# Performance work log

Hardware: AMD Instinct MI355X
Metric: run time of the kernel (lower is better)

The kernel has to match this reference:

```python
import jax, jax.numpy as jnp
import numpy as np
from jax import lax


def setup_inputs() -> dict:
    key = jax.random.key(0)
    ks = jax.random.split(key, 16)
    def rn(k, shape, s=0.05):
        return (jax.random.normal(k, shape) * s).astype(jnp.float32)
    B, N, F = 16, 1024, 200
    return dict(
        x=jax.random.normal(ks[0], (B, 1, N, F), dtype=jnp.float32),
        gat_W=rn(ks[1], (F, F)), att_src=rn(ks[2], (F,)), att_dst=rn(ks[3], (F,)), gat_b=rn(ks[4], (F,)),
        conv1_w=rn(ks[5], (40, 1, 1, 26)), conv1_b=rn(ks[6], (40,)),
        bn1_g=jnp.ones((40,), jnp.float32), bn1_b=jnp.zeros((40,), jnp.float32),
        bn1_m=jnp.zeros((40,), jnp.float32), bn1_v=jnp.ones((40,), jnp.float32),
        conv2_w=rn(ks[7], (40, 40, N), 0.01), conv2_b=rn(ks[8], (40,)),
        bn2_g=jnp.ones((40,), jnp.float32), bn2_b=jnp.zeros((40,), jnp.float32),
        bn2_m=jnp.zeros((40,), jnp.float32), bn2_v=jnp.ones((40,), jnp.float32),
        projc_w=rn(ks[9], (40, 40)), projc_b=rn(ks[10], (40,)),
        W1=rn(ks[11], (1400, 1024)), b1=rn(ks[12], (1024,)),
        W2=rn(ks[13], (1024, 1024)), b2=rn(ks[14], (1024,)),
        ln_g=jnp.ones((1024,), jnp.float32), ln_b=jnp.zeros((1024,), jnp.float32),
    )


def _bn(y, g, b, m, v, eps=1e-5):
    # eval-mode BatchNorm over channel axis 1
    shp = (1, -1) + (1,) * (y.ndim - 2)
    return (y - m.reshape(shp)) * (g.reshape(shp) / jnp.sqrt(v.reshape(shp) + eps)) + b.reshape(shp)


def reference(x, gat_W, att_src, att_dst, gat_b, conv1_w, conv1_b,
              bn1_g, bn1_b, bn1_m, bn1_v, conv2_w, conv2_b,
              bn2_g, bn2_b, bn2_m, bn2_v, projc_w, projc_b,
              W1, b1, W2, b2, ln_g, ln_b):
    B, _, N, F = x.shape  # (16,1,1024,200)
    # --- EEG_GAT (PyG GATConv, heads=1). edge_index only covers nodes 0..N-1;
    # add_self_loops applies to all B*N nodes -> first graph is dense attention
    # (complete graph incl. self), remaining nodes see only their self-loop.
    h = x.reshape(B * N, F) @ gat_W               # (B*N, 200)
    a_s = h[:N] @ att_src                          # source scores, first graph
    a_d = h[:N] @ att_dst                          # target scores
    logits = jax.nn.leaky_relu(a_s[None, :] + a_d[:, None], 0.2)  # [target i, source j]
    out0 = jax.nn.softmax(logits, axis=1) @ h[:N]  # (N, 200)
    gat = (jnp.concatenate([out0, h[N:]], axis=0) + gat_b).reshape(B, 1, N, F)
    x = x + gat  # ResidualAdd (dropout in eval = identity)
    # --- PatchEmbedding shallownet
    y = lax.conv_general_dilated(x, conv1_w, (1, 1), 'VALID',
                                 dimension_numbers=('NCHW', 'OIHW', 'NCHW'))
    y = y + conv1_b[None, :, None, None]           # (B,40,1024,175)
    y = y.reshape(B, 40, N, 35, 5).mean(-1)        # AvgPool2d (1,5) stride (1,5)
    y = jax.nn.elu(_bn(y, bn1_g, bn1_b, bn1_m, bn1_v))
    y = jnp.einsum('bchw,och->bow', y, conv2_w) + conv2_b[None, :, None]  # Conv2d(40,40,(1024,1)) -> (B,40,35)
    y = jax.nn.elu(_bn(y, bn2_g, bn2_b, bn2_m, bn2_v))
    # projection 1x1 conv then rearrange 'b e h w -> b (h w) e' then flatten
    y = jnp.einsum('bow,eo->bew', y, projc_w) + projc_b[None, :, None]
    y = y.transpose(0, 2, 1).reshape(B, -1)        # (B, 1400)
    # --- Proj_eeg
    z = y @ W1 + b1
    z = z + (jax.nn.gelu(z, approximate=False) @ W2 + b2)
    mu = z.mean(-1, keepdims=True)
    var = ((z - mu) ** 2).mean(-1, keepdims=True)
    return (z - mu) / jnp.sqrt(var + 1e-5) * ln_g + ln_b
```

## Files before the change

kernel.cpp:

```cpp
#include <hip/hip_runtime.h>
#include <math.h>

typedef __attribute__((ext_vector_type(8))) short short8;
typedef __attribute__((ext_vector_type(4))) float f32x4;

__device__ __forceinline__ unsigned f2bf(float f) {
  unsigned u = __float_as_uint(f);
  return (u + 0x7FFFu + ((u >> 16) & 1u)) >> 16;
}
__device__ __forceinline__ unsigned pk2(float lo, float hi) {
  return f2bf(lo) | (f2bf(hi) << 16);
}

#define WS_X1    0
#define WS_W2P   3328000
#define WS_AS    4966400
#define WS_AD    4967424
#define WS_WEFF  4968464
#define WS_S1    4969664
#define WS_SH1   4969704
#define WS_S2    4969744
#define WS_SH2   4969784
#define WS_H     4970496
#define WS_P     5232640
#define WS_AP    6281216
#define WS_Y3P   WS_P
#define WS_Y4    8378368
#define WS_Y5    8400768
#define WS_ZP    8455936
#define WS_Z2P   8570624
#define WS_WPT   8701696

__global__ __launch_bounds__(256) void k0_prep(const float* __restrict__ gat_W,
                        const float* __restrict__ conv1_w, const float* __restrict__ conv1_b,
                        const float* __restrict__ bn1_g, const float* __restrict__ bn1_b,
                        const float* __restrict__ bn1_m, const float* __restrict__ bn1_v,
                        const float* __restrict__ conv2_b,
                        const float* __restrict__ bn2_g, const float* __restrict__ bn2_b,
                        const float* __restrict__ bn2_m, const float* __restrict__ bn2_v,
                        const float* __restrict__ w2,
                        float* __restrict__ ws) {
  int bx = blockIdx.x, t = threadIdx.x;
  if (bx < 224) {
    unsigned short* wpt = (unsigned short*)(ws + WS_WPT);
    int idx = bx * 256 + t;
    int n = idx / 224, k = idx % 224;
    float v = (n < 200 && k < 200) ? gat_W[k * 200 + n] : 0.f;
    wpt[idx] = (unsigned short)f2bf(v);
    return;
  }
  if (bx == 224) {
    if (t < 40) {
      float* weff = ws + WS_WEFF;
      for (int j = 0; j < 30; ++j) {
        float s = 0.f;
        for (int tt = 0; tt < 5; ++tt) {
          int k = j - tt;
          if (k >= 0 && k < 26) s += conv1_w[t * 26 + k];
        }
        weff[t * 30 + j] = s * 0.2f;
      }
      float s1 = bn1_g[t] * rsqrtf(bn1_v[t] + 1e-5f);
      ws[WS_S1 + t] = s1;
      ws[WS_SH1 + t] = bn1_b[t] + (conv1_b[t] - bn1_m[t]) * s1;
      float s2 = bn2_g[t] * rsqrtf(bn2_v[t] + 1e-5f);
      ws[WS_S2 + t] = s2;
      ws[WS_SH2 + t] = bn2_b[t] + (conv2_b[t] - bn2_m[t]) * s2;
    }
    return;
  }
  int idx = (bx - 225) * 256 + t;
  if (idx < 1966080) {
    unsigned short* w2p = (unsigned short*)(ws + WS_W2P);
    int k = idx % 320;
    int rem = idx / 320;
    int o = rem % 48, c8 = rem / 48;
    float v = 0.f;
    if (o < 40) {
      int c = k % 40, nl = k / 40;
      v = w2[(o * 40 + c) * 1024 + c8 * 8 + nl];
    }
    w2p[idx] = (unsigned short)f2bf(v);
  }
}

__global__ __launch_bounds__(256) void k1_mfma(const float* __restrict__ x,
                                               const unsigned short* __restrict__ wpt,
                                               const float* __restrict__ gat_b,
                                               float* __restrict__ h,
                                               float* __restrict__ x1) {
  __shared__ unsigned short Bt[64 * 232];
  __shared__ unsigned short As[2][64 * 40];
  int t = threadIdx.x;
  int wave = t >> 6, lane = t & 63;
  int m16 = lane & 15, quad = lane >> 4;
  int row0 = blockIdx.x * 64, n0 = blockIdx.y * 64;
  for (int i = t; i < 1792; i += 256) {
    int row = i / 28, ch = i % 28;
    *(short8*)&Bt[row * 232 + ch * 8] = *(const short8*)&wpt[(n0 + row) * 224 + ch * 8];
  }
  {
    int m = t >> 2, kq = (t & 3) * 8;
    const float* xr = x + (row0 + m) * 200 + kq;
    float4 a = *(const float4*)xr;
    float4 b = *(const float4*)(xr + 4);
    uint4 pv;
    pv.x = pk2(a.x, a.y); pv.y = pk2(a.z, a.w);
    pv.z = pk2(b.x, b.y); pv.w = pk2(b.z, b.w);
    *(uint4*)&As[0][m * 40 + kq] = pv;
  }
  __syncthreads();
  f32x4 acc0 = {0.f, 0.f, 0.f, 0.f}, acc1 = acc0, acc2 = acc0, acc3 = acc0;
  int buf = 0;
  for (int s = 0; s < 7; ++s) {
    if (s < 6) {
      int m = t >> 2, kq = (t & 3) * 8;
      int kg = (s + 1) * 32 + kq;
      const float* xr = x + (row0 + m) * 200;
      uint4 pv;
      if (kg + 8 <= 200) {
        float4 a = *(const float4*)(xr + kg);
        float4 b = *(const float4*)(xr + kg + 4);
        pv.x = pk2(a.x, a.y); pv.y = pk2(a.z, a.w);
        pv.z = pk2(b.x, b.y); pv.w = pk2(b.z, b.w);
      } else {
        float e[8];
#pragma unroll
        for (int q = 0; q < 8; ++q) e[q] = (kg + q < 200) ? xr[kg + q] : 0.f;
        pv.x = pk2(e[0], e[1]); pv.y = pk2(e[2], e[3]);
        pv.z = pk2(e[4], e[5]); pv.w = pk2(e[6], e[7]);
      }
      *(uint4*)&As[buf ^ 1][m * 40 + kq] = pv;
    }
    short8 af = *(const short8*)&As[buf][(wave * 16 + m16) * 40 + quad * 8];
    int kb = s * 32 + quad * 8;
    short8 b0 = *(const short8*)&Bt[(0 * 16 + m16) * 232 + kb];
    short8 b1 = *(const short8*)&Bt[(1 * 16 + m16) * 232 + kb];
    short8 b2 = *(const short8*)&Bt[(2 * 16 + m16) * 232 + kb];
    short8 b3 = *(const short8*)&Bt[(3 * 16 + m16) * 232 + kb];
    acc0 = __builtin_amdgcn_mfma_f32_16x16x32_bf16(af, b0, acc0, 0, 0, 0);
    acc1 = __builtin_amdgcn_mfma_f32_16x16x32_bf16(af, b1, acc1, 0, 0, 0);
    acc2 = __builtin_amdgcn_mfma_f32_16x16x32_bf16(af, b2, acc2, 0, 0, 0);
    acc3 = __builtin_amdgcn_mfma_f32_16x16x32_bf16(af, b3, acc3, 0, 0, 0);
    __syncthreads();
    buf ^= 1;
  }
  f32x4 accs[4] = {acc0, acc1, acc2, acc3};
  if (blockIdx.x < 16) {
#pragma unroll
    for (int nt = 0; nt < 4; ++nt)
#pragma unroll
      for (int r = 0; r < 4; ++r) {
        int row = row0 + wave * 16 + quad * 4 + r;
        h[row * 256 + n0 + nt * 16 + m16] = accs[nt][r];
      }
  } else {
#pragma unroll
    for (int nt = 0; nt < 4; ++nt) {
      int col = n0 + nt * 16 + m16;
      if (col < 200) {
#pragma unroll
        for (int r = 0; r < 4; ++r) {
          int row = row0 + wave * 16 + quad * 4 + r;
          x1[row * 200 + col] = x[row * 200 + col] + accs[nt][r] + gat_b[col];
        }
      }
    }
  }
}

__global__ void k1b_scores(const float* __restrict__ h, const float* __restrict__ att_src,
                           const float* __restrict__ att_dst, float* __restrict__ as_,
                           float* __restrict__ ad_) {
  int r = blockIdx.x * 256 + threadIdx.x;
  const float* hr = h + r * 256;
  float s = 0.f, d = 0.f;
  for (int f = 0; f < 200; ++f) {
    float v = hr[f];
    s += v * att_src[f];
    d += v * att_dst[f];
  }
  as_[r] = s;
  ad_[r] = d;
}

__global__ __launch_bounds__(256) void kP(const float* __restrict__ as_,
                                          const float* __restrict__ ad_,
                                          float* __restrict__ P) {
  __shared__ float rb[256];
  int t = threadIdx.x, i = blockIdx.x;
  float a0 = as_[t], a1 = as_[256 + t], a2 = as_[512 + t], a3 = as_[768 + t];
  rb[t] = fmaxf(fmaxf(a0, a1), fmaxf(a2, a3));
  __syncthreads();
  for (int st = 128; st > 0; st >>= 1) {
    if (t < st) rb[t] = fmaxf(rb[t], rb[t + st]);
    __syncthreads();
  }
  float maxs = rb[0];
  __syncthreads();
  float ad = ad_[i];
  float mv = maxs + ad;
  float M = mv >= 0.f ? mv : 0.2f * mv;
  float av[4] = {a0, a1, a2, a3};
  float p[4];
  float s = 0.f;
#pragma unroll
  for (int q = 0; q < 4; ++q) {
    float v = av[q] + ad;
    float l = v >= 0.f ? v : 0.2f * v;
    p[q] = __expf(l - M);
    s += p[q];
  }
  rb[t] = s;
  __syncthreads();
  for (int st = 128; st > 0; st >>= 1) {
    if (t < st) rb[t] += rb[t + st];
    __syncthreads();
  }
  float inv = 1.f / rb[0];
#pragma unroll
  for (int q = 0; q < 4; ++q) P[i * 1024 + q * 256 + t] = p[q] * inv;
}

__global__ __launch_bounds__(256) void kAttn(const float* __restrict__ P,
                                             const float* __restrict__ h,
                                             float* __restrict__ ap) {
  __shared__ __align__(16) float As2[8][64];
  __shared__ __align__(16) float Bs[8][64];
  int t = threadIdx.x;
  int tm = t & 15, tn = t >> 4;
  int i0 = blockIdx.x * 64, f0 = blockIdx.y * 64, j0 = blockIdx.z * 128;
  float acc[4][4] = {};
  for (int k0 = 0; k0 < 128; k0 += 8) {
    for (int i = t; i < 512; i += 256) {
      int m = i >> 3, k = i & 7;
      As2[k][m] = P[(i0 + m) * 1024 + j0 + k0 + k];
    }
    for (int i = t; i < 512; i += 256) {
      int k = i >> 6, n = i & 63;
      Bs[k][n] = h[(j0 + k0 + k) * 256 + f0 + n];
    }
    __syncthreads();
#pragma unroll
    for (int k = 0; k < 8; ++k) {
      float4 a = *(const float4*)&As2[k][tm * 4];
      float4 bq = *(const float4*)&Bs[k][tn * 4];
      float av[4] = {a.x, a.y, a.z, a.w};
      float bv[4] = {bq.x, bq.y, bq.z, bq.w};
#pragma unroll
      for (int i = 0; i < 4; ++i)
#pragma unroll
        for (int j = 0; j < 4; ++j) acc[i][j] += av[i] * bv[j];
    }
    __syncthreads();
  }
#pragma unroll
  for (int i = 0; i < 4; ++i) {
    int r = i0 + tm * 4 + i;
    float4 v = make_float4(acc[i][0], acc[i][1], acc[i][2], acc[i][3]);
    *(float4*)&ap[(blockIdx.z * 1024 + r) * 256 + f0 + tn * 4] = v;
  }
}

__global__ __launch_bounds__(256) void kAttnRed(const float* __restrict__ ap,
                                                const float* __restrict__ x,
                                                const float* __restrict__ gat_b,
                                                float* __restrict__ x1) {
  int t = threadIdx.x, r = blockIdx.x;
  if (t >= 200) return;
  float s = 0.f;
#pragma unroll
  for (int z = 0; z < 8; ++z) s += ap[(z * 1024 + r) * 256 + t];
  x1[r * 200 + t] = x[r * 200 + t] + s + gat_b[t];
}

__global__ __launch_bounds__(320, 2) void k3_conv(const float* __restrict__ x1,
                                                  const unsigned short* __restrict__ w2pre,
                                                  const float* __restrict__ ws,
                                                  float* __restrict__ y3p) {
  __shared__ __align__(16) char smem[33856];
  float* xbp = (float*)smem;
  unsigned short* tmpA = (unsigned short*)(smem + 10240);
  int t = threadIdx.x;
  int b = blockIdx.x, nc = blockIdx.y;
  int n0 = nc * 8;
  int wave = t >> 6, lane = t & 63;
  int l15 = lane & 15, quad = lane >> 4;
  for (int i = t; i < 400; i += 320) {
    int nn = i / 50, q = i % 50;
    float4 v = ((const float4*)(x1 + (b * 1024 + n0 + nn) * 200))[q];
    float vv[4] = {v.x, v.y, v.z, v.w};
#pragma unroll
    for (int m = 0; m < 4; ++m) {
      int j = q * 4 + m;
      xbp[nn * 320 + (j / 5) * 8 + (j % 5)] = vv[m];
    }
  }
  int c1 = t / 7, wg = t % 7;
  float wr[30];
  float s1c = 0.f, sh1c = 0.f;
  if (t < 280) {
    const float* weff = ws + WS_WEFF + c1 * 30;
#pragma unroll
    for (int j = 0; j < 30; ++j) wr[j] = weff[j];
    s1c = ws[WS_S1 + c1];
    sh1c = ws[WS_SH1 + c1];
  }
  __syncthreads();
  if (t < 280) {
    for (int nn = 0; nn < 8; ++nn) {
      float xq[10][5];
      int xb = nn * 320 + wg * 40;
#pragma unroll
      for (int pi = 0; pi < 10; ++pi) {
        float4 v = *(const float4*)&xbp[xb + pi * 8];
        xq[pi][0] = v.x; xq[pi][1] = v.y; xq[pi][2] = v.z; xq[pi][3] = v.w;
        xq[pi][4] = xbp[xb + pi * 8 + 4];
      }
#pragma unroll
      for (int u = 0; u < 5; ++u) {
        float s = 0.f;
#pragma unroll
        for (int m = 0; m < 6; ++m)
#pragma unroll
          for (int r = 0; r < 5; ++r) s += xq[u + m][r] * wr[m * 5 + r];
        float v = s * s1c + sh1c;
        float e = v > 0.f ? v : __expf(v) - 1.f;
        tmpA[(wg * 5 + u) * 328 + nn * 40 + c1] = (unsigned short)f2bf(e);
      }
    }
  }
  __syncthreads();
  f32x4 acc[3][3];
#pragma unroll
  for (int mt = 0; mt < 3; ++mt)
#pragma unroll
    for (int nt = 0; nt < 3; ++nt) acc[mt][nt] = (f32x4){0.f, 0.f, 0.f, 0.f};
  const unsigned short* bbase = w2pre + nc * 48 * 320;
#pragma unroll
  for (int ks = 0; ks < 2; ++ks) {
    int koff = wave * 64 + ks * 32 + quad * 8;
    short8 a[3], bb[3];
#pragma unroll
    for (int mt = 0; mt < 3; ++mt) {
      int row = mt * 16 + l15;
      row = row > 35 ? 35 : row;
      a[mt] = *(const short8*)&tmpA[row * 328 + koff];
    }
#pragma unroll
    for (int nt = 0; nt < 3; ++nt)
      bb[nt] = *(const short8*)&bbase[(nt * 16 + l15) * 320 + koff];
#pragma unroll
    for (int mt = 0; mt < 3; ++mt)
#pragma unroll
      for (int nt = 0; nt < 3; ++nt)
        acc[mt][nt] = __builtin_amdgcn_mfma_f32_16x16x32_bf16(a[mt], bb[nt], acc[mt][nt], 0, 0, 0);
  }
  __syncthreads();
  float* red0 = (float*)smem;
  float* red1 = red0 + 48 * 49;
  if (wave < 2) {
    float* r = wave ? red1 : red0;
#pragma unroll
    for (int mt = 0; mt < 3; ++mt)
#pragma unroll
      for (int nt = 0; nt < 3; ++nt)
#pragma unroll
        for (int q = 0; q < 4; ++q)
          r[(mt * 16 + quad * 4 + q) * 49 + nt * 16 + l15] = acc[mt][nt][q];
  }
  __syncthreads();
  if (wave == 2 || wave == 3) {
    float* r = (wave == 3) ? red1 : red0;
#pragma unroll
    for (int mt = 0; mt < 3; ++mt)
#pragma unroll
      for (int nt = 0; nt < 3; ++nt)
#pragma unroll
        for (int q = 0; q < 4; ++q)
          r[(mt * 16 + quad * 4 + q) * 49 + nt * 16 + l15] += acc[mt][nt][q];
  }
  __syncthreads();
  if (wave == 4) {
#pragma unroll
    for (int mt = 0; mt < 3; ++mt)
#pragma unroll
      for (int nt = 0; nt < 3; ++nt)
#pragma unroll
        for (int q = 0; q < 4; ++q)
          red0[(mt * 16 + quad * 4 + q) * 49 + nt * 16 + l15] += acc[mt][nt][q];
  }
  __syncthreads();
  float* dst = y3p + (b * 128 + nc) * 1400;
  for (int idx = t; idx < 1400; idx += 320) {
    int o = idx / 35, p = idx % 35;
    dst[idx] = red0[p * 49 + o] + red1[p * 49 + o];
  }
}

__global__ __launch_bounds__(256) void k4a_red(const float* __restrict__ y3p,
                                               const float* __restrict__ ws,
                                               float* __restrict__ y4) {
  int t = threadIdx.x;
  if (t >= 200) return;
  int b = blockIdx.x;
  int idx = blockIdx.y * 200 + t;
  float s = 0.f;
#pragma unroll 4
  for (int q = 0; q < 128; ++q) s += y3p[(b * 128 + q) * 1400 + idx];
  int o = idx / 35;
  float v = s * ws[WS_S2 + o] + ws[WS_SH2 + o];
  y4[b * 1400 + idx] = v > 0.f ? v : __expf(v) - 1.f;
}

__global__ __launch_bounds__(256) void k4b_proj(const float* __restrict__ y4,
                                                const float* __restrict__ projc_w,
                                                const float* __restrict__ projc_b,
                                                float* __restrict__ y5) {
  __shared__ __align__(16) float tls[1400];
  int t = threadIdx.x, b = blockIdx.x;
  for (int i = t; i < 350; i += 256)
    ((float4*)tls)[i] = ((const float4*)(y4 + b * 1400))[i];
  __syncthreads();
  for (int idx = t; idx < 1400; idx += 256) {
    int p = idx / 40, e = idx % 40;
    float acc = projc_b[e];
    for (int o = 0; o < 40; ++o) acc += tls[o * 35 + p] * projc_w[e * 40 + o];
    y5[b * 1400 + idx] = acc;
  }
}

__global__ __launch_bounds__(256) void k5_fc1(const float* __restrict__ y5,
                                              const float* __restrict__ W1,
                                              float* __restrict__ zp) {
  __shared__ __align__(16) float yls[3200];
  int t = threadIdx.x;
  int nc = blockIdx.x, kc = blockIdx.y;
  for (int i = t; i < 800; i += 256) {
    int bb = i / 50, q = i % 50;
    ((float4*)yls)[bb * 50 + q] = *(const float4*)(y5 + bb * 1400 + kc * 200 + q * 4);
  }
  __syncthreads();
  int nl = t & 31, bg = t >> 5;
  int n = nc * 32 + nl;
  float acc0 = 0.f, acc1 = 0.f;
  const float* y0 = yls + (bg * 2) * 200;
  const float* y1 = yls + (bg * 2 + 1) * 200;
  for (int k = 0; k < 200; ++k) {
    float w = W1[(kc * 200 + k) * 1024 + n];
    acc0 += y0[k] * w;
    acc1 += y1[k] * w;
  }
  zp[(kc * 16 + bg * 2) * 1024 + n] = acc0;
  zp[(kc * 16 + bg * 2 + 1) * 1024 + n] = acc1;
}

__global__ __launch_bounds__(256) void k6_fc2(const float* __restrict__ zp,
                                              const float* __restrict__ b1,
                                              const float* __restrict__ W2,
                                              float* __restrict__ z2p) {
  __shared__ __align__(16) float gls[2048];
  int t = threadIdx.x;
  int nc = blockIdx.x, kc = blockIdx.y;
  for (int i = t; i < 2048; i += 256) {
    int bb = i >> 7, kk = i & 127;
    int np = kc * 128 + kk;
    float s = b1[np];
#pragma unroll
    for (int j = 0; j < 7; ++j) s += zp[(j * 16 + bb) * 1024 + np];
    gls[i] = 0.5f * s * (1.f + erff(s * 0.70710678f));
  }
  __syncthreads();
  int nl = t & 31, bg = t >> 5;
  int n = nc * 32 + nl;
  float acc0 = 0.f, acc1 = 0.f;
  const float* g0 = gls + (bg * 2) * 128;
  const float* g1 = gls + (bg * 2 + 1) * 128;
  for (int k = 0; k < 128; ++k) {
    float w = W2[(kc * 128 + k) * 1024 + n];
    acc0 += g0[k] * w;
    acc1 += g1[k] * w;
  }
  z2p[(kc * 16 + bg * 2) * 1024 + n] = acc0;
  z2p[(kc * 16 + bg * 2 + 1) * 1024 + n] = acc1;
}

__global__ __launch_bounds__(256) void k7_ln(const float* __restrict__ zp,
                                             const float* __restrict__ z2p,
                                             const float* __restrict__ b1,
                                             const float* __restrict__ b2,
                                             const float* __restrict__ ln_g,
                                             const float* __restrict__ ln_b,
                                             float* __restrict__ out) {
  __shared__ float r1[256], r2[256];
  int t = threadIdx.x, b = blockIdx.x;
  float4 v = *(const float4*)(b1 + t * 4);
  float4 bb2 = *(const float4*)(b2 + t * 4);
  v.x += bb2.x; v.y += bb2.y; v.z += bb2.z; v.w += bb2.w;
#pragma unroll
  for (int kc = 0; kc < 7; ++kc) {
    float4 p = *(const float4*)(zp + (kc * 16 + b) * 1024 + t * 4);
    v.x += p.x; v.y += p.y; v.z += p.z; v.w += p.w;
  }
#pragma unroll
  for (int kc = 0; kc < 8; ++kc) {
    float4 p = *(const float4*)(z2p + (kc * 16 + b) * 1024 + t * 4);
    v.x += p.x; v.y += p.y; v.z += p.z; v.w += p.w;
  }
  r1[t] = v.x + v.y + v.z + v.w;
  r2[t] = v.x * v.x + v.y * v.y + v.z * v.z + v.w * v.w;
  __syncthreads();
  for (int s = 128; s > 0; s >>= 1) {
    if (t < s) {
      r1[t] += r1[t + s];
      r2[t] += r2[t + s];
    }
    __syncthreads();
  }
  float mu = r1[0] * (1.f / 1024.f);
  float var = r2[0] * (1.f / 1024.f) - mu * mu;
  float rstd = rsqrtf(var + 1e-5f);
  float4 gg = *(const float4*)(ln_g + t * 4);
  float4 bb = *(const float4*)(ln_b + t * 4);
  float4 o;
  o.x = (v.x - mu) * rstd * gg.x + bb.x;
  o.y = (v.y - mu) * rstd * gg.y + bb.y;
  o.z = (v.z - mu) * rstd * gg.z + bb.z;
  o.w = (v.w - mu) * rstd * gg.w + bb.w;
  *(float4*)(out + b * 1024 + t * 4) = o;
}

extern "C" void kernel_launch(void* const* d_in, const int* in_sizes, int n_in,
                              void* d_out, int out_size, void* d_ws, size_t ws_size,
                              hipStream_t stream) {
  (void)in_sizes; (void)n_in; (void)out_size; (void)ws_size;
  const float* x       = (const float*)d_in[0];
  const float* gat_W   = (const float*)d_in[1];
  const float* att_src = (const float*)d_in[2];
  const float* att_dst = (const float*)d_in[3];
  const float* gat_b   = (const float*)d_in[4];
  const float* conv1_w = (const float*)d_in[5];
  const float* conv2_w = (const float*)d_in[11];
  const float* projc_w = (const float*)d_in[17];
  const float* projc_b = (const float*)d_in[18];
  const float* W1      = (const float*)d_in[19];
  const float* b1      = (const float*)d_in[20];
  const float* W2      = (const float*)d_in[21];
  const float* b2      = (const float*)d_in[22];
  const float* ln_g    = (const float*)d_in[23];
  const float* ln_b    = (const float*)d_in[24];
  float* ws  = (float*)d_ws;
  float* out = (float*)d_out;

  hipLaunchKernelGGL(k0_prep, dim3(7905), dim3(256), 0, stream, gat_W, conv1_w,
                     (const float*)d_in[6], (const float*)d_in[7], (const float*)d_in[8],
                     (const float*)d_in[9], (const float*)d_in[10], (const float*)d_in[12],
                     (const float*)d_in[13], (const float*)d_in[14], (const float*)d_in[15],
                     (const float*)d_in[16], conv2_w, ws);
  hipLaunchKernelGGL(k1_mfma, dim3(256, 4), dim3(256), 0, stream, x,
                     (const unsigned short*)(ws + WS_WPT), gat_b, ws + WS_H, ws + WS_X1);
  hipLaunchKernelGGL(k1b_scores, dim3(4), dim3(256), 0, stream, ws + WS_H, att_src, att_dst,
                     ws + WS_AS, ws + WS_AD);
  hipLaunchKernelGGL(kP, dim3(1024), dim3(256), 0, stream, ws + WS_AS, ws + WS_AD, ws + WS_P);
  hipLaunchKernelGGL(kAttn, dim3(16, 4, 8), dim3(256), 0, stream, ws + WS_P, ws + WS_H,
                     ws + WS_AP);
  hipLaunchKernelGGL(kAttnRed, dim3(1024), dim3(256), 0, stream, ws + WS_AP, x, gat_b,
                     ws + WS_X1);
  hipLaunchKernelGGL(k3_conv, dim3(16, 128), dim3(320), 0, stream, ws + WS_X1,
                     (const unsigned short*)(ws + WS_W2P), ws, ws + WS_Y3P);
  hipLaunchKernelGGL(k4a_red, dim3(16, 7), dim3(256), 0, stream, ws + WS_Y3P, ws, ws + WS_Y4);
  hipLaunchKernelGGL(k4b_proj, dim3(16), dim3(256), 0, stream, ws + WS_Y4, projc_w, projc_b,
                     ws + WS_Y5);
  hipLaunchKernelGGL(k5_fc1, dim3(32, 7), dim3(256), 0, stream, ws + WS_Y5, W1, ws + WS_ZP);
  hipLaunchKernelGGL(k6_fc2, dim3(32, 8), dim3(256), 0, stream, ws + WS_ZP, b1, W2,
                     ws + WS_Z2P);
  hipLaunchKernelGGL(k7_ln, dim3(16), dim3(256), 0, stream, ws + WS_ZP, ws + WS_Z2P, b1, b2,
                     ln_g, ln_b, out);
}
```

Before: 280.4 us.

## Use MFMA for conv1 stage, coalesce W2 prep, parallelize attention scores

The conv1+avgpool+BN+ELU stage in k3_conv is recast as a bf16 MFMA GEMM. Each pooled output window is built as a 30-wide (padded to 32) im2col row, and the effective conv weights are prepacked to bf16 in k0_prep. The conv2 weight repack in k0_prep now goes through LDS, so writes are coalesced and far fewer blocks are launched. k1b_scores uses one wave per row with float4 loads and shuffle reductions instead of one thread per row over only 4 blocks. These changes cut scalar FMA work and latency-bound kernels, at the cost of more LDS per conv block and bf16 rounding of the conv1 inputs and weights.

```diff
diff --git a/kernel.cpp b/kernel.cpp
--- a/kernel.cpp
+++ b/kernel.cpp
@@ -16,7 +16,7 @@
 #define WS_W2P   3328000
 #define WS_AS    4966400
 #define WS_AD    4967424
-#define WS_WEFF  4968464
+#define WS_WEFB  4968464
 #define WS_S1    4969664
 #define WS_SH1   4969704
 #define WS_S2    4969744
@@ -50,16 +50,23 @@
     return;
   }
   if (bx == 224) {
+    if (t < 48) {
+      unsigned short* wb = (unsigned short*)(ws + WS_WEFB);
+      float wv[30];
+      if (t < 40) {
+        for (int j = 0; j < 30; ++j) {
+          float s = 0.f;
+          for (int tt = 0; tt < 5; ++tt) {
+            int k = j - tt;
+            if (k >= 0 && k < 26) s += conv1_w[t * 26 + k];
+          }
+          wv[j] = s * 0.2f;
+        }
+      }
+      for (int k = 0; k < 32; ++k)
+        wb[t * 32 + k] = (unsigned short)f2bf((t < 40 && k < 30) ? wv[k] : 0.f);
+    }
     if (t < 40) {
-      float* weff = ws + WS_WEFF;
-      for (int j = 0; j < 30; ++j) {
-        float s = 0.f;
-        for (int tt = 0; tt < 5; ++tt) {
-          int k = j - tt;
-          if (k >= 0 && k < 26) s += conv1_w[t * 26 + k];
-        }
-        weff[t * 30 + j] = s * 0.2f;
-      }
       float s1 = bn1_g[t] * rsqrtf(bn1_v[t] + 1e-5f);
       ws[WS_S1 + t] = s1;
       ws[WS_SH1 + t] = bn1_b[t] + (conv1_b[t] - bn1_m[t]) * s1;
@@ -69,19 +76,23 @@
     }
     return;
   }
-  int idx = (bx - 225) * 256 + t;
-  if (idx < 1966080) {
-    unsigned short* w2p = (unsigned short*)(ws + WS_W2P);
-    int k = idx % 320;
-    int rem = idx / 320;
-    int o = rem % 48, c8 = rem / 48;
-    float v = 0.f;
-    if (o < 40) {
-      int c = k % 40, nl = k / 40;
-      v = w2[(o * 40 + c) * 1024 + c8 * 8 + nl];
-    }
-    w2p[idx] = (unsigned short)f2bf(v);
-  }
+  __shared__ unsigned short lds[2560];
+  int q = bx - 225;
+  int c8 = q / 6, o0 = (q % 6) * 8;
+  unsigned short* w2p = (unsigned short*)(ws + WS_W2P);
+#pragma unroll
+  for (int i = 0; i < 10; ++i) {
+    int e = i * 256 + t;
+    int o = e / 320, rr = e % 320;
+    int c = rr / 8, nl = rr % 8;
+    int oa = o0 + o;
+    float v = (oa < 40) ? w2[(oa * 40 + c) * 1024 + c8 * 8 + nl] : 0.f;
+    lds[o * 320 + nl * 40 + c] = (unsigned short)f2bf(v);
+  }
+  __syncthreads();
+  uint4* src = (uint4*)lds;
+  uint4* dst = (uint4*)(w2p + (c8 * 48 + o0) * 320);
+  for (int i = t; i < 320; i += 256) dst[i] = src[i];
 }
 
 __global__ __launch_bounds__(256) void k1_mfma(const float* __restrict__ x,
@@ -169,19 +180,31 @@
   }
 }
 
-__global__ void k1b_scores(const float* __restrict__ h, const float* __restrict__ att_src,
-                           const float* __restrict__ att_dst, float* __restrict__ as_,
-                           float* __restrict__ ad_) {
-  int r = blockIdx.x * 256 + threadIdx.x;
-  const float* hr = h + r * 256;
+__global__ __launch_bounds__(256) void k1b_scores(const float* __restrict__ h,
+                                                  const float* __restrict__ att_src,
+                                                  const float* __restrict__ att_dst,
+                                                  float* __restrict__ as_,
+                                                  float* __restrict__ ad_) {
+  int t = threadIdx.x;
+  int wave = t >> 6, lane = t & 63;
+  int r = blockIdx.x * 4 + wave;
   float s = 0.f, d = 0.f;
-  for (int f = 0; f < 200; ++f) {
-    float v = hr[f];
-    s += v * att_src[f];
-    d += v * att_dst[f];
-  }
-  as_[r] = s;
-  ad_[r] = d;
+  if (lane < 50) {
+    float4 v = *(const float4*)(h + r * 256 + lane * 4);
+    float4 a = *(const float4*)(att_src + lane * 4);
+    float4 dd = *(const float4*)(att_dst + lane * 4);
+    s = v.x * a.x + v.y * a.y + v.z * a.z + v.w * a.w;
+    d = v.x * dd.x + v.y * dd.y + v.z * dd.z + v.w * dd.w;
+  }
+#pragma unroll
+  for (int off = 32; off > 0; off >>= 1) {
+    s += __shfl_down(s, off);
+    d += __shfl_down(d, off);
+  }
+  if (lane == 0) {
+    as_[r] = s;
+    ad_[r] = d;
+  }
 }
 
 __global__ __launch_bounds__(256) void kP(const float* __restrict__ as_,
@@ -276,11 +299,13 @@
 
 __global__ __launch_bounds__(320, 2) void k3_conv(const float* __restrict__ x1,
                                                   const unsigned short* __restrict__ w2pre,
+                                                  const unsigned short* __restrict__ weffB,
                                                   const float* __restrict__ ws,
                                                   float* __restrict__ y3p) {
-  __shared__ __align__(16) char smem[33856];
+  __shared__ __align__(16) char smem[48448];
   float* xbp = (float*)smem;
-  unsigned short* tmpA = (unsigned short*)(smem + 10240);
+  unsigned short* tA = (unsigned short*)(smem + 6400);
+  unsigned short* t2 = (unsigned short*)(smem + 24832);
   int t = threadIdx.x;
   int b = blockIdx.x, nc = blockIdx.y;
   int n0 = nc * 8;
@@ -288,45 +313,60 @@
   int l15 = lane & 15, quad = lane >> 4;
   for (int i = t; i < 400; i += 320) {
     int nn = i / 50, q = i % 50;
-    float4 v = ((const float4*)(x1 + (b * 1024 + n0 + nn) * 200))[q];
-    float vv[4] = {v.x, v.y, v.z, v.w};
-#pragma unroll
-    for (int m = 0; m < 4; ++m) {
-      int j = q * 4 + m;
-      xbp[nn * 320 + (j / 5) * 8 + (j % 5)] = vv[m];
-    }
-  }
-  int c1 = t / 7, wg = t % 7;
-  float wr[30];
-  float s1c = 0.f, sh1c = 0.f;
+    ((float4*)(xbp + nn * 200))[q] = ((const float4*)(x1 + (b * 1024 + n0 + nn) * 200))[q];
+  }
+  __syncthreads();
   if (t < 280) {
-    const float* weff = ws + WS_WEFF + c1 * 30;
-#pragma unroll
-    for (int j = 0; j < 30; ++j) wr[j] = weff[j];
-    s1c = ws[WS_S1 + c1];
-    sh1c = ws[WS_SH1 + c1];
-  }
-  __syncthreads();
-  if (t < 280) {
-    for (int nn = 0; nn < 8; ++nn) {
-      float xq[10][5];
-      int xb = nn * 320 + wg * 40;
-#pragma unroll
-      for (int pi = 0; pi < 10; ++pi) {
-        float4 v = *(const float4*)&xbp[xb + pi * 8];
-        xq[pi][0] = v.x; xq[pi][1] = v.y; xq[pi][2] = v.z; xq[pi][3] = v.w;
-        xq[pi][4] = xbp[xb + pi * 8 + 4];
+    int nn = t / 35, p = t % 35;
+    const float* xr = xbp + nn * 200 + p * 5;
+    uint pv[16];
+#pragma unroll
+    for (int kk = 0; kk < 15; ++kk) pv[kk] = pk2(xr[kk * 2], xr[kk * 2 + 1]);
+    pv[15] = 0u;
+    uint4* dst = (uint4*)(tA + t * 32);
+    dst[0] = make_uint4(pv[0], pv[1], pv[2], pv[3]);
+    dst[1] = make_uint4(pv[4], pv[5], pv[6], pv[7]);
+    dst[2] = make_uint4(pv[8], pv[9], pv[10], pv[11]);
+    dst[3] = make_uint4(pv[12], pv[13], pv[14], pv[15]);
+  } else if (t < 288) {
+    uint4 z = make_uint4(0u, 0u, 0u, 0u);
+    uint4* dst = (uint4*)(tA + t * 32);
+    dst[0] = z; dst[1] = z; dst[2] = z; dst[3] = z;
+  }
+  __syncthreads();
+  {
+    int mt0 = wave * 4;
+    int nmt = wave < 4 ? 4 : 2;
+    short8 bw[3];
+    float s1v[3] = {0.f, 0.f, 0.f}, sh1v[3] = {0.f, 0.f, 0.f};
+#pragma unroll
+    for (int nt = 0; nt < 3; ++nt) {
+      bw[nt] = *(const short8*)&weffB[(nt * 16 + l15) * 32 + quad * 8];
+      int c = nt * 16 + l15;
+      if (c < 40) {
+        s1v[nt] = ws[WS_S1 + c];
+        sh1v[nt] = ws[WS_SH1 + c];
       }
-#pragma unroll
-      for (int u = 0; u < 5; ++u) {
-        float s = 0.f;
-#pragma unroll
-        for (int m = 0; m < 6; ++m)
-#pragma unroll
-          for (int r = 0; r < 5; ++r) s += xq[u + m][r] * wr[m * 5 + r];
-        float v = s * s1c + sh1c;
-        float e = v > 0.f ? v : __expf(v) - 1.f;
-        tmpA[(wg * 5 + u) * 328 + nn * 40 + c1] = (unsigned short)f2bf(e);
+    }
+    for (int mi = 0; mi < nmt; ++mi) {
+      int mt = mt0 + mi;
+      short8 a = *(const short8*)&tA[(mt * 16 + l15) * 32 + quad * 8];
+#pragma unroll
+      for (int nt = 0; nt < 3; ++nt) {
+        int c = nt * 16 + l15;
+        if (c >= 40) continue;
+        f32x4 c4 = {0.f, 0.f, 0.f, 0.f};
+        c4 = __builtin_amdgcn_mfma_f32_16x16x32_bf16(a, bw[nt], c4, 0, 0, 0);
+#pragma unroll
+        for (int r = 0; r < 4; ++r) {
+          int m = mt * 16 + quad * 4 + r;
+          if (m < 280) {
+            float v = c4[r] * s1v[nt] + sh1v[nt];
+            float e = v > 0.f ? v : __expf(v) - 1.f;
+            int p = m % 35, nn = m / 35;
+            t2[p * 328 + nn * 40 + c] = (unsigned short)f2bf(e);
+          }
+        }
       }
     }
   }
@@ -345,7 +385,7 @@
     for (int mt = 0; mt < 3; ++mt) {
       int row = mt * 16 + l15;
       row = row > 35 ? 35 : row;
-      a[mt] = *(const short8*)&tmpA[row * 328 + koff];
+      a[mt] = *(const short8*)&t2[row * 328 + koff];
     }
 #pragma unroll
     for (int nt = 0; nt < 3; ++nt)
@@ -552,14 +592,14 @@
   float* ws  = (float*)d_ws;
   float* out = (float*)d_out;
 
-  hipLaunchKernelGGL(k0_prep, dim3(7905), dim3(256), 0, stream, gat_W, conv1_w,
+  hipLaunchKernelGGL(k0_prep, dim3(993), dim3(256), 0, stream, gat_W, conv1_w,
                      (const float*)d_in[6], (const float*)d_in[7], (const float*)d_in[8],
                      (const float*)d_in[9], (const float*)d_in[10], (const float*)d_in[12],
                      (const float*)d_in[13], (const float*)d_in[14], (const float*)d_in[15],
                      (const float*)d_in[16], conv2_w, ws);
   hipLaunchKernelGGL(k1_mfma, dim3(256, 4), dim3(256), 0, stream, x,
                      (const unsigned short*)(ws + WS_WPT), gat_b, ws + WS_H, ws + WS_X1);
-  hipLaunchKernelGGL(k1b_scores, dim3(4), dim3(256), 0, stream, ws + WS_H, att_src, att_dst,
+  hipLaunchKernelGGL(k1b_scores, dim3(256), dim3(256), 0, stream, ws + WS_H, att_src, att_dst,
                      ws + WS_AS, ws + WS_AD);
   hipLaunchKernelGGL(kP, dim3(1024), dim3(256), 0, stream, ws + WS_AS, ws + WS_AD, ws + WS_P);
   hipLaunchKernelGGL(kAttn, dim3(16, 4, 8), dim3(256), 0, stream, ws + WS_P, ws + WS_H,
@@ -567,7 +607,8 @@
   hipLaunchKernelGGL(kAttnRed, dim3(1024), dim3(256), 0, stream, ws + WS_AP, x, gat_b,
                      ws + WS_X1);
   hipLaunchKernelGGL(k3_conv, dim3(16, 128), dim3(320), 0, stream, ws + WS_X1,
-                     (const unsigned short*)(ws + WS_W2P), ws, ws + WS_Y3P);
+                     (const unsigned short*)(ws + WS_W2P),
+                     (const unsigned short*)(ws + WS_WEFB), ws, ws + WS_Y3P);
   hipLaunchKernelGGL(k4a_red, dim3(16, 7), dim3(256), 0, stream, ws + WS_Y3P, ws, ws + WS_Y4);
   hipLaunchKernelGGL(k4b_proj, dim3(16), dim3(256), 0, stream, ws + WS_Y4, projc_w, projc_b,
                      ws + WS_Y5);
```

After: 245.6 us. 12.4% less time.
